# Optimization experiments

Hardware: AMD Instinct MI355X
Metric: run time of the kernel (lower is better)

The kernel has to match this reference:

```python
import jax, jax.numpy as jnp
import numpy as np
from jax import lax

LAMBDA_REG = 0.01


def setup_inputs() -> dict:
    key = jax.random.key(0)
    k1, k2 = jax.random.split(key)
    features = jax.random.normal(k1, (8192, 512), dtype=jnp.float32)
    attention_scores = jax.random.uniform(k2, (8192,), dtype=jnp.float32)
    return {"features": features, "attention_scores": attention_scores, "k": 256}


def _kernel_matrix(features, attention_scores, lambda_reg=LAMBDA_REG):
    # L_ij = sqrt(q_i q_j) * <f_i, f_j>/(|f_i||f_j|) + lambda * I
    fn = features / jnp.linalg.norm(features, axis=1, keepdims=True)
    S = fn @ fn.T                                   # [N, N] cosine similarity
    q = attention_scores
    L = jnp.sqrt(q[:, None] * q[None, :]) * S
    N = features.shape[0]
    return L + lambda_reg * jnp.eye(N, dtype=features.dtype)


def _greedy_map(L, k):
    # Fast greedy DPP MAP (Chen et al. 2018): incremental Cholesky.
    # Marginal log-det gain of adding item i to selected set Y is log d_i,
    # where d_i = L_ii - ||c_i||^2 is the Schur complement. argmax over d_i
    # equals argmax over logdet(L_{Y+i}) since logdet(L_{Y+i}) = logdet(L_Y) + log d_i.
    N = L.shape[0]

    def step(carry, t):
        d, cis, mask = carry                         # d:[N], cis:[k,N], mask:[N]
        j = jnp.argmax(jnp.where(mask, d, -jnp.inf))  # first max (matches torch '>' tie-break)
        # e_n = (L[j,n] - sum_t cis[t,j]*cis[t,n]) / sqrt(d_j); unused rows of cis are zero
        e = (L[j] - cis[:, j] @ cis) / jnp.sqrt(d[j])  # [N]
        cis = cis.at[t].set(e)
        return (d - e * e, cis, mask.at[j].set(False)), j

    init = (jnp.diagonal(L), jnp.zeros((k, N), L.dtype), jnp.ones(N, dtype=bool))
    _, idx = lax.scan(step, init, jnp.arange(k))
    return idx                                        # [k] int selected indices


def reference(features, attention_scores, k):
    L = _kernel_matrix(features, attention_scores)
    return _greedy_map(L, k)
```

## Files before the change

### kernel.cpp

```cpp
#include <hip/hip_runtime.h>
#include <math.h>
#include <stdint.h>


#define N 8192
#define D 512
#define K 256
#define LAMBDA_REG 0.01f
#define NBLK 256
#define NTHR 256
#define ROWS 32
#define RS   560
#define CS   68
#define CTS  264
#define SSTR 8
#define SCOPE __HIP_MEMORY_SCOPE_AGENT

typedef unsigned long long u64;
typedef float f32x4 __attribute__((ext_vector_type(4)));

struct __align__(8) Pick { float v; int i; };

__device__ __forceinline__ bool better(float av, int ai, float bv, int bi) {
    return (av > bv) || (av == bv && ai < bi);
}

__device__ __forceinline__ u64 pack_slot(float v, int idx, int tag) {
    unsigned hi = ((unsigned)tag << 13) | (unsigned)idx;
    return ((u64)hi << 32) | (u64)__float_as_uint(v);
}

__device__ __forceinline__ void bypass_store_u64(u64* p, u64 v) {
    asm volatile("global_store_dwordx2 %0, %1, off sc0 sc1"
                 :: "v"(p), "v"(v) : "memory");
}

__device__ __forceinline__ void bypass_store_f32x4(const f32x4* p, f32x4 v) {
    asm volatile("global_store_dwordx4 %0, %1, off sc0 sc1"
                 :: "v"(p), "v"(v) : "memory");
}

__global__ __launch_bounds__(NTHR, 1) void dpp_kernel(
        const float* __restrict__ F, const float* __restrict__ q,
        float* __restrict__ FN, float* __restrict__ cisT,
        u64* __restrict__ slots, int* __restrict__ out)
{
    const int tid = threadIdx.x;
    const int blk = blockIdx.x;
    const int r   = tid >> 3;
    const int c   = tid & 7;
    const int n   = blk * ROWS + r;

    __shared__ __align__(16) float lds_fn[ROWS * RS];
    __shared__ __align__(16) float lds_ct[ROWS * CTS];
    __shared__ __align__(16) float lds_gj[8 * CS];
    __shared__ __align__(16) float lds_cj[K];
    __shared__ Pick lds_wave[NTHR / 64];
    __shared__ Pick lds_final;

    const f32x4* F4  = reinterpret_cast<const f32x4*>(F);
    f32x4*       FN4 = reinterpret_cast<f32x4*>(FN);

    float dloc, qn;
    bool  masked = false;
    {
        const f32x4* src = F4 + (size_t)n * (D / 4) + c * 16;
        float* frow = &lds_fn[r * RS + c * CS];
        float ss = 0.f;
        #pragma unroll
        for (int i = 0; i < 16; ++i) {
            f32x4 v = src[i];
            *reinterpret_cast<f32x4*>(frow + 4 * i) = v;
            ss = fmaf(v.x, v.x, ss); ss = fmaf(v.y, v.y, ss);
            ss = fmaf(v.z, v.z, ss); ss = fmaf(v.w, v.w, ss);
        }
        ss += __shfl_xor(ss, 1); ss += __shfl_xor(ss, 2); ss += __shfl_xor(ss, 4);
        const float norm = sqrtf(ss);
        f32x4* dst = FN4 + (size_t)n * (D / 4) + c * 16;
        float ssn = 0.f;
        #pragma unroll
        for (int i = 0; i < 16; ++i) {
            f32x4 v = *reinterpret_cast<f32x4*>(frow + 4 * i);
            v.x /= norm; v.y /= norm; v.z /= norm; v.w /= norm;
            *reinterpret_cast<f32x4*>(frow + 4 * i) = v;
            bypass_store_f32x4(dst + i, v);
            ssn = fmaf(v.x, v.x, ssn); ssn = fmaf(v.y, v.y, ssn);
            ssn = fmaf(v.z, v.z, ssn); ssn = fmaf(v.w, v.w, ssn);
        }
        ssn += __shfl_xor(ssn, 1); ssn += __shfl_xor(ssn, 2); ssn += __shfl_xor(ssn, 4);
        qn = q[n];
        dloc = fmaf(sqrtf(qn * qn), ssn, LAMBDA_REG);
    }

    {
        float v = dloc; int idx = n;
        #pragma unroll
        for (int m = 32; m > 0; m >>= 1) {
            float ov = __shfl_xor(v, m);
            int   oi = __shfl_xor(idx, m);
            if (better(ov, oi, v, idx)) { v = ov; idx = oi; }
        }
        if ((tid & 63) == 0) { lds_wave[tid >> 6].v = v; lds_wave[tid >> 6].i = idx; }
        asm volatile("s_waitcnt vmcnt(0)" ::: "memory");
        __syncthreads();
        if (tid == 0) {
            Pick p = lds_wave[0];
            #pragma unroll
            for (int w = 1; w < NTHR / 64; ++w) {
                Pick o = lds_wave[w];
                if (better(o.v, o.i, p.v, p.i)) p = o;
            }
            bypass_store_u64(&slots[blk * SSTR], pack_slot(p.v, p.i, 0));
        }
    }

    for (int t = 0; t < K; ++t) {
        const unsigned want = (unsigned)t;

        if (tid < 64) {
            const u64* pb = slots + (t & 1) * NBLK * SSTR;
            u64 x0, x1, x2, x3;
            while (true) {
                x0 = __hip_atomic_load(pb + (tid * 4 + 0) * SSTR, __ATOMIC_RELAXED, SCOPE);
                x1 = __hip_atomic_load(pb + (tid * 4 + 1) * SSTR, __ATOMIC_RELAXED, SCOPE);
                x2 = __hip_atomic_load(pb + (tid * 4 + 2) * SSTR, __ATOMIC_RELAXED, SCOPE);
                x3 = __hip_atomic_load(pb + (tid * 4 + 3) * SSTR, __ATOMIC_RELAXED, SCOPE);
                bool ok = ((unsigned)(x0 >> 45) == want) &&
                          ((unsigned)(x1 >> 45) == want) &&
                          ((unsigned)(x2 >> 45) == want) &&
                          ((unsigned)(x3 >> 45) == want);
                if (__all(ok)) break;
                __builtin_amdgcn_s_sleep(1);
            }
            asm volatile("" ::: "memory");
            float v = __uint_as_float((unsigned)x0);
            int idx = (int)((x0 >> 32) & 8191u);
            {
                float w = __uint_as_float((unsigned)x1); int k1 = (int)((x1 >> 32) & 8191u);
                if (better(w, k1, v, idx)) { v = w; idx = k1; }
                w = __uint_as_float((unsigned)x2); k1 = (int)((x2 >> 32) & 8191u);
                if (better(w, k1, v, idx)) { v = w; idx = k1; }
                w = __uint_as_float((unsigned)x3); k1 = (int)((x3 >> 32) & 8191u);
                if (better(w, k1, v, idx)) { v = w; idx = k1; }
            }
            #pragma unroll
            for (int m = 32; m > 0; m >>= 1) {
                float ov = __shfl_xor(v, m);
                int   oi = __shfl_xor(idx, m);
                if (better(ov, oi, v, idx)) { v = ov; idx = oi; }
            }
            if (tid == 0) { lds_final.v = v; lds_final.i = idx; }
        }
        __syncthreads();
        const float dj = lds_final.v;
        const int   j  = lds_final.i;

        if (blk == 0 && tid == 0) out[t] = j;
        if (t == K - 1) break;

        const float sj = sqrtf(dj);
        const float qj = q[j];

        f32x4 gv;
        float cv0, cv1;
        int   tt0 = tid - 128, tt1 = tid;
        if (tid < 128) {
            gv = FN4[(size_t)j * (D / 4) + tid];
        } else {
            if (tt0 < t) cv0 = cisT[(size_t)j * K + tt0];
            if (tt1 < t) cv1 = cisT[(size_t)j * K + tt1];
        }
        if (tid < 128) {
            *reinterpret_cast<f32x4*>(&lds_gj[(tid >> 4) * CS + (tid & 15) * 4]) = gv;
        } else {
            if (tt0 < t) lds_cj[tt0] = cv0;
            if (tt1 < t) lds_cj[tt1] = cv1;
        }
        __syncthreads();

        const float* frow = &lds_fn[r * RS + c * CS];
        const float* grow = &lds_gj[c * CS];
        f32x4 a = {0.f, 0.f, 0.f, 0.f};
        #pragma unroll
        for (int i = 0; i < 16; ++i) {
            f32x4 v = *reinterpret_cast<const f32x4*>(frow + 4 * i);
            f32x4 g = *reinterpret_cast<const f32x4*>(grow + 4 * i);
            a.x = fmaf(v.x, g.x, a.x); a.y = fmaf(v.y, g.y, a.y);
            a.z = fmaf(v.z, g.z, a.z); a.w = fmaf(v.w, g.w, a.w);
        }
        float dot = (a.x + a.y) + (a.z + a.w);
        dot += __shfl_xor(dot, 1); dot += __shfl_xor(dot, 2); dot += __shfl_xor(dot, 4);
        float Ljn = sqrtf(qj * qn) * dot;
        if (n == j) Ljn += LAMBDA_REG;

        float cd = 0.f;
        const float* ctrow = &lds_ct[r * CTS];
        for (int tt = c; tt < t; tt += 8)
            cd = fmaf(lds_cj[tt], ctrow[tt], cd);
        cd += __shfl_xor(cd, 1); cd += __shfl_xor(cd, 2); cd += __shfl_xor(cd, 4);

        const float e = (Ljn - cd) / sj;
        if (c == 0) {
            lds_ct[r * CTS + t] = e;
            const float* ep = cisT + (size_t)n * K + t;
            asm volatile("global_store_dword %0, %1, off sc0 sc1"
                         :: "v"(ep), "v"(e) : "memory");
        }
        dloc = fmaf(-e, e, dloc);
        if (n == j) masked = true;

        {
            float v = masked ? -INFINITY : dloc; int idx = n;
            #pragma unroll
            for (int m = 32; m > 0; m >>= 1) {
                float ov = __shfl_xor(v, m);
                int   oi = __shfl_xor(idx, m);
                if (better(ov, oi, v, idx)) { v = ov; idx = oi; }
            }
            if ((tid & 63) == 0) { lds_wave[tid >> 6].v = v; lds_wave[tid >> 6].i = idx; }
        }
        asm volatile("s_waitcnt lgkmcnt(0)" ::: "memory");
        __builtin_amdgcn_sched_barrier(0);
        __builtin_amdgcn_s_barrier();
        __builtin_amdgcn_sched_barrier(0);
        if (tid == 0) {
            Pick p = lds_wave[0];
            #pragma unroll
            for (int w = 1; w < NTHR / 64; ++w) {
                Pick o = lds_wave[w];
                if (better(o.v, o.i, p.v, p.i)) p = o;
            }
            bypass_store_u64(&slots[(((t + 1) & 1) * NBLK + blk) * SSTR],
                             pack_slot(p.v, p.i, t + 1));
        }
    }
}

extern "C" void kernel_launch(void* const* d_in, const int* in_sizes, int n_in,
                              void* d_out, int out_size, void* d_ws, size_t ws_size,
                              hipStream_t stream) {
    const float* F = (const float*)d_in[0];
    const float* q = (const float*)d_in[1];
    int* out = (int*)d_out;

    uint8_t* w = (uint8_t*)d_ws;
    u64*   slots = (u64*)(w + 4096);
    float* FN    = (float*)(w + 131072);
    float* cisT  = (float*)(w + 131072 + (size_t)N * D * 4);

    hipMemsetAsync((void*)w, 0xFF, 65536, stream);
    hipLaunchKernelGGL(dpp_kernel, dim3(NBLK), dim3(NTHR), 0, stream,
                       F, q, FN, cisT, slots, out);
}
```

Measured before the change: 1.182 ms.

## Use 64 blocks of 1024 threads and read normalized features from global memory

Reshapes the persistent kernel from 256 blocks of 256 threads to 64 blocks of 1024 threads, each covering 128 rows. The per-iteration inter-block argmax poll shrinks to one slot per lane, cutting the global spin-wait and reduction work. The LDS copy of the normalized feature rows is removed, so each step's dot product re-reads the rows from global memory (FN), relying on cache hits. The trade is fewer blocks to synchronize against repeated global loads each iteration and larger intra-block barriers.

```diff
diff --git a/kernel.cpp b/kernel.cpp
--- a/kernel.cpp
+++ b/kernel.cpp
@@ -7,10 +7,9 @@
 #define D 512
 #define K 256
 #define LAMBDA_REG 0.01f
-#define NBLK 256
-#define NTHR 256
-#define ROWS 32
-#define RS   560
+#define NBLK 64
+#define NTHR 1024
+#define ROWS 128
 #define CS   68
 #define CTS  264
 #define SSTR 8
@@ -40,18 +39,19 @@
                  :: "v"(p), "v"(v) : "memory");
 }
 
-__global__ __launch_bounds__(NTHR, 1) void dpp_kernel(
+__global__ __launch_bounds__(NTHR, 4) void dpp_kernel(
         const float* __restrict__ F, const float* __restrict__ q,
         float* __restrict__ FN, float* __restrict__ cisT,
         u64* __restrict__ slots, int* __restrict__ out)
 {
-    const int tid = threadIdx.x;
-    const int blk = blockIdx.x;
-    const int r   = tid >> 3;
-    const int c   = tid & 7;
-    const int n   = blk * ROWS + r;
-
-    __shared__ __align__(16) float lds_fn[ROWS * RS];
+    const int tid  = threadIdx.x;
+    const int blk  = blockIdx.x;
+    const int wid  = tid >> 6;
+    const int lane = tid & 63;
+    const int r    = tid >> 3;
+    const int c    = tid & 7;
+    const int n    = blk * ROWS + r;
+
     __shared__ __align__(16) float lds_ct[ROWS * CTS];
     __shared__ __align__(16) float lds_gj[8 * CS];
     __shared__ __align__(16) float lds_cj[K];
@@ -65,12 +65,10 @@
     bool  masked = false;
     {
         const f32x4* src = F4 + (size_t)n * (D / 4) + c * 16;
-        float* frow = &lds_fn[r * RS + c * CS];
         float ss = 0.f;
-        #pragma unroll
+        #pragma unroll 4
         for (int i = 0; i < 16; ++i) {
             f32x4 v = src[i];
-            *reinterpret_cast<f32x4*>(frow + 4 * i) = v;
             ss = fmaf(v.x, v.x, ss); ss = fmaf(v.y, v.y, ss);
             ss = fmaf(v.z, v.z, ss); ss = fmaf(v.w, v.w, ss);
         }
@@ -78,11 +76,10 @@
         const float norm = sqrtf(ss);
         f32x4* dst = FN4 + (size_t)n * (D / 4) + c * 16;
         float ssn = 0.f;
-        #pragma unroll
+        #pragma unroll 4
         for (int i = 0; i < 16; ++i) {
-            f32x4 v = *reinterpret_cast<f32x4*>(frow + 4 * i);
+            f32x4 v = src[i];
             v.x /= norm; v.y /= norm; v.z /= norm; v.w /= norm;
-            *reinterpret_cast<f32x4*>(frow + 4 * i) = v;
             bypass_store_f32x4(dst + i, v);
             ssn = fmaf(v.x, v.x, ssn); ssn = fmaf(v.y, v.y, ssn);
             ssn = fmaf(v.z, v.z, ssn); ssn = fmaf(v.w, v.w, ssn);
@@ -100,7 +97,7 @@
             int   oi = __shfl_xor(idx, m);
             if (better(ov, oi, v, idx)) { v = ov; idx = oi; }
         }
-        if ((tid & 63) == 0) { lds_wave[tid >> 6].v = v; lds_wave[tid >> 6].i = idx; }
+        if (lane == 0) { lds_wave[wid].v = v; lds_wave[wid].i = idx; }
         asm volatile("s_waitcnt vmcnt(0)" ::: "memory");
         __syncthreads();
         if (tid == 0) {
@@ -119,30 +116,15 @@
 
         if (tid < 64) {
             const u64* pb = slots + (t & 1) * NBLK * SSTR;
-            u64 x0, x1, x2, x3;
+            u64 x;
             while (true) {
-                x0 = __hip_atomic_load(pb + (tid * 4 + 0) * SSTR, __ATOMIC_RELAXED, SCOPE);
-                x1 = __hip_atomic_load(pb + (tid * 4 + 1) * SSTR, __ATOMIC_RELAXED, SCOPE);
-                x2 = __hip_atomic_load(pb + (tid * 4 + 2) * SSTR, __ATOMIC_RELAXED, SCOPE);
-                x3 = __hip_atomic_load(pb + (tid * 4 + 3) * SSTR, __ATOMIC_RELAXED, SCOPE);
-                bool ok = ((unsigned)(x0 >> 45) == want) &&
-                          ((unsigned)(x1 >> 45) == want) &&
-                          ((unsigned)(x2 >> 45) == want) &&
-                          ((unsigned)(x3 >> 45) == want);
-                if (__all(ok)) break;
+                x = __hip_atomic_load(pb + tid * SSTR, __ATOMIC_RELAXED, SCOPE);
+                if (__all((unsigned)(x >> 45) == want)) break;
                 __builtin_amdgcn_s_sleep(1);
             }
             asm volatile("" ::: "memory");
-            float v = __uint_as_float((unsigned)x0);
-            int idx = (int)((x0 >> 32) & 8191u);
-            {
-                float w = __uint_as_float((unsigned)x1); int k1 = (int)((x1 >> 32) & 8191u);
-                if (better(w, k1, v, idx)) { v = w; idx = k1; }
-                w = __uint_as_float((unsigned)x2); k1 = (int)((x2 >> 32) & 8191u);
-                if (better(w, k1, v, idx)) { v = w; idx = k1; }
-                w = __uint_as_float((unsigned)x3); k1 = (int)((x3 >> 32) & 8191u);
-                if (better(w, k1, v, idx)) { v = w; idx = k1; }
-            }
+            float v = __uint_as_float((unsigned)x);
+            int idx = (int)((x >> 32) & 8191u);
             #pragma unroll
             for (int m = 32; m > 0; m >>= 1) {
                 float ov = __shfl_xor(v, m);
@@ -161,29 +143,21 @@
         const float sj = sqrtf(dj);
         const float qj = q[j];
 
-        f32x4 gv;
-        float cv0, cv1;
-        int   tt0 = tid - 128, tt1 = tid;
         if (tid < 128) {
-            gv = FN4[(size_t)j * (D / 4) + tid];
-        } else {
-            if (tt0 < t) cv0 = cisT[(size_t)j * K + tt0];
-            if (tt1 < t) cv1 = cisT[(size_t)j * K + tt1];
-        }
-        if (tid < 128) {
+            f32x4 gv = FN4[(size_t)j * (D / 4) + tid];
             *reinterpret_cast<f32x4*>(&lds_gj[(tid >> 4) * CS + (tid & 15) * 4]) = gv;
-        } else {
-            if (tt0 < t) lds_cj[tt0] = cv0;
-            if (tt1 < t) lds_cj[tt1] = cv1;
+        } else if (tid >= 256 && tid < 512) {
+            const int tt = tid - 256;
+            if (tt < t) lds_cj[tt] = cisT[(size_t)j * K + tt];
         }
         __syncthreads();
 
-        const float* frow = &lds_fn[r * RS + c * CS];
+        const f32x4* ow = FN4 + (size_t)n * (D / 4) + c * 16;
         const float* grow = &lds_gj[c * CS];
         f32x4 a = {0.f, 0.f, 0.f, 0.f};
-        #pragma unroll
+        #pragma unroll 4
         for (int i = 0; i < 16; ++i) {
-            f32x4 v = *reinterpret_cast<const f32x4*>(frow + 4 * i);
+            f32x4 v = ow[i];
             f32x4 g = *reinterpret_cast<const f32x4*>(grow + 4 * i);
             a.x = fmaf(v.x, g.x, a.x); a.y = fmaf(v.y, g.y, a.y);
             a.z = fmaf(v.z, g.z, a.z); a.w = fmaf(v.w, g.w, a.w);
@@ -217,7 +191,7 @@
                 int   oi = __shfl_xor(idx, m);
                 if (better(ov, oi, v, idx)) { v = ov; idx = oi; }
             }
-            if ((tid & 63) == 0) { lds_wave[tid >> 6].v = v; lds_wave[tid >> 6].i = idx; }
+            if (lane == 0) { lds_wave[wid].v = v; lds_wave[wid].i = idx; }
         }
         asm volatile("s_waitcnt lgkmcnt(0)" ::: "memory");
         __builtin_amdgcn_sched_barrier(0);
```

Measured after the change: 2.910 ms. +146.1%, slower.
